# Kernel tuning notes

Measured on AMD Instinct MI355X. Metric: run time of the kernel, lower is better.

Reference implementation:

```python
import jax, jax.numpy as jnp
import numpy as np

T, N, H, I = 128, 1024, 512, 64


def _orthogonal(key, shape, dtype=jnp.float32):
    # mimic torch nn.init.orthogonal_ on a [rows, cols] matrix
    rows, cols = shape
    a = jax.random.normal(key, (max(rows, cols), min(rows, cols)), dtype=jnp.float32)
    q, r = jnp.linalg.qr(a)
    q = q * jnp.sign(jnp.diag(r))
    if rows < cols:
        q = q.T
    return q[:rows, :cols].astype(dtype)


def setup_inputs() -> dict:
    key = jax.random.key(0)
    k1, k2, k3, k4, k5, k6 = jax.random.split(key, 6)
    hxs = jax.random.normal(k1, (N, H), dtype=jnp.float32)
    gru_init = jax.random.normal(k2, (T * N, H), dtype=jnp.float32)
    masks = jax.random.uniform(k3, (T * N, 1), dtype=jnp.float32)
    prev_action_one_hot = jax.random.normal(k4, (T, N, I), dtype=jnp.float32)
    # GRUCell params: weight_ih [3H, I], weight_hh [3H, H] (orthogonal init), zero biases
    W_ih = _orthogonal(k5, (3 * H, I))
    W_hh = _orthogonal(k6, (3 * H, H))
    b_ih = jnp.zeros((3 * H,), dtype=jnp.float32)
    b_hh = jnp.zeros((3 * H,), dtype=jnp.float32)
    return {"hxs": hxs, "gru_init": gru_init, "masks": masks,
            "prev_action_one_hot": prev_action_one_hot,
            "W_ih": W_ih, "W_hh": W_hh, "b_ih": b_ih, "b_hh": b_hh}


def _gru_cell(x, h, W_ih, W_hh, b_ih, b_hh):
    # PyTorch GRUCell math; gate order in weights is r, z, n
    gi = x @ W_ih.T + b_ih          # [N, 3H]
    gh = h @ W_hh.T + b_hh          # [N, 3H]
    i_r, i_z, i_n = jnp.split(gi, 3, axis=-1)
    h_r, h_z, h_n = jnp.split(gh, 3, axis=-1)
    r = jax.nn.sigmoid(i_r + h_r)
    z = jax.nn.sigmoid(i_z + h_z)
    n = jnp.tanh(i_n + r * h_n)
    return (1.0 - z) * n + z * h


def reference(hxs, gru_init, masks, prev_action_one_hot, W_ih, W_hh, b_ih, b_hh):
    n = hxs.shape[0]
    t = gru_init.shape[0] // n
    m = masks.reshape(t, n, 1)
    # NOTE: the original computes hxs*m + gru_init*(1-m) per step but never uses it
    # (dead code), so gru_init does not enter the output.

    def step(h, inp):
        mi, xi = inp
        h_new = _gru_cell(xi * mi, h * mi, W_ih, W_hh, b_ih, b_hh)
        return h_new, h_new

    h_final, outs = jax.lax.scan(step, hxs, (m, prev_action_one_hot))
    x = outs.reshape(t * n, -1)
    return x, h_final
```

## Files before the change

### kernel.cpp

```cpp
#include <hip/hip_runtime.h>


#define T_STEPS 128
#define NBATCH  1024
#define HDIM    512
#define IDIM    64
#define KTOT    576
#define BM      64
#define BN      32
#define LDP     40

typedef _Float16 half8  __attribute__((ext_vector_type(8)));
typedef float    floatx4 __attribute__((ext_vector_type(4)));

__global__ void prep_w_kernel(const float* __restrict__ Whh,
                              const float* __restrict__ Wih,
                              _Float16* __restrict__ W16) {
    int idx = blockIdx.x * 256 + threadIdx.x;
    if (idx >= 1536 * KTOT) return;
    int c = idx / KTOT;
    int k = idx - c * KTOT;
    float v = (k < HDIM) ? Whh[c * HDIM + k] : Wih[c * IDIM + (k - HDIM)];
    W16[idx] = (_Float16)v;
}

__device__ __forceinline__ float sigmoidf_(float x) {
    return 1.0f / (1.0f + __expf(-x));
}

__global__ __launch_bounds__(256)
void gru_step_kernel(const float* __restrict__ h_prev,
                     const float* __restrict__ x_t,
                     const float* __restrict__ m_t,
                     const _Float16* __restrict__ W16,
                     const float* __restrict__ b_ih,
                     const float* __restrict__ b_hh,
                     float* __restrict__ out_x,
                     float* __restrict__ out_h) {
    __shared__ __align__(16) _Float16 As[BM * LDP];
    __shared__ __align__(16) _Float16 Bs[3][BN * LDP];

    const int tid = threadIdx.x;
    const int rt = blockIdx.x >> 4;
    const int ctile = blockIdx.x & 15;
    const int rowbase = rt * BM;
    const int colbase = ctile * BN;

    const int arow = tid >> 2;
    const int ak0  = (tid & 3) * 8;
    const float maskv = m_t[rowbase + arow];

    const int wave = tid >> 6;
    const int lane = tid & 63;
    const int n16  = lane & 15;
    const int q    = lane >> 4;

    floatx4 acc_r[2], acc_z[2], acc_hn[2], acc_in[2];
#pragma unroll
    for (int bt = 0; bt < 2; ++bt) {
        acc_r[bt] = (floatx4){0.f, 0.f, 0.f, 0.f};
        acc_z[bt] = (floatx4){0.f, 0.f, 0.f, 0.f};
        acc_hn[bt] = (floatx4){0.f, 0.f, 0.f, 0.f};
        acc_in[bt] = (floatx4){0.f, 0.f, 0.f, 0.f};
    }

    for (int kt = 0; kt < 18; ++kt) {
        const int kbase = kt * 32;

        const float* asrc;
        if (kt < 16) {
            asrc = h_prev + (size_t)(rowbase + arow) * HDIM + kbase + ak0;
        } else {
            asrc = x_t + (size_t)(rowbase + arow) * IDIM + (kbase - HDIM) + ak0;
        }
        floatx4 a0 = *(const floatx4*)asrc;
        floatx4 a1 = *(const floatx4*)(asrc + 4);
        half8 av;
        av[0] = (_Float16)(a0.x * maskv);
        av[1] = (_Float16)(a0.y * maskv);
        av[2] = (_Float16)(a0.z * maskv);
        av[3] = (_Float16)(a0.w * maskv);
        av[4] = (_Float16)(a1.x * maskv);
        av[5] = (_Float16)(a1.y * maskv);
        av[6] = (_Float16)(a1.z * maskv);
        av[7] = (_Float16)(a1.w * maskv);
        *(half8*)&As[arow * LDP + ak0] = av;

#pragma unroll
        for (int ii = 0; ii < 2; ++ii) {
            int idx = tid + ii * 256;
            if (idx < 384) {
                int g    = idx >> 7;
                int rem  = idx & 127;
                int brow = rem >> 2;
                int bk0  = (rem & 3) * 8;
                const _Float16* bsrc =
                    W16 + (size_t)(g * HDIM + colbase + brow) * KTOT + kbase + bk0;
                *(half8*)&Bs[g][brow * LDP + bk0] = *(const half8*)bsrc;
            }
        }
        __syncthreads();

        half8 af = *(const half8*)&As[(wave * 16 + n16) * LDP + q * 8];
#pragma unroll
        for (int bt = 0; bt < 2; ++bt) {
            half8 br = *(const half8*)&Bs[0][(bt * 16 + n16) * LDP + q * 8];
            half8 bz = *(const half8*)&Bs[1][(bt * 16 + n16) * LDP + q * 8];
            half8 bn = *(const half8*)&Bs[2][(bt * 16 + n16) * LDP + q * 8];
            acc_r[bt] = __builtin_amdgcn_mfma_f32_16x16x32_f16(af, br, acc_r[bt], 0, 0, 0);
            acc_z[bt] = __builtin_amdgcn_mfma_f32_16x16x32_f16(af, bz, acc_z[bt], 0, 0, 0);
            if (kt < 16) {
                acc_hn[bt] = __builtin_amdgcn_mfma_f32_16x16x32_f16(af, bn, acc_hn[bt], 0, 0, 0);
            } else {
                acc_in[bt] = __builtin_amdgcn_mfma_f32_16x16x32_f16(af, bn, acc_in[bt], 0, 0, 0);
            }
        }
        __syncthreads();
    }

#pragma unroll
    for (int bt = 0; bt < 2; ++bt) {
        const int c = colbase + bt * 16 + n16;
        const float brb = b_ih[c] + b_hh[c];
        const float bzb = b_ih[c + HDIM] + b_hh[c + HDIM];
        const float bin = b_ih[c + 2 * HDIM];
        const float bhn = b_hh[c + 2 * HDIM];
#pragma unroll
        for (int r = 0; r < 4; ++r) {
            const int i = rowbase + wave * 16 + q * 4 + r;
            const float rg = sigmoidf_(acc_r[bt][r] + brb);
            const float zg = sigmoidf_(acc_z[bt][r] + bzb);
            const float ng = tanhf(acc_in[bt][r] + bin + rg * (acc_hn[bt][r] + bhn));
            const float hm = h_prev[(size_t)i * HDIM + c] * m_t[i];
            const float hv = (1.0f - zg) * ng + zg * hm;
            out_x[(size_t)i * HDIM + c] = hv;
            if (out_h) out_h[(size_t)i * HDIM + c] = hv;
        }
    }
}

extern "C" void kernel_launch(void* const* d_in, const int* in_sizes, int n_in,
                              void* d_out, int out_size, void* d_ws, size_t ws_size,
                              hipStream_t stream) {
    const float* hxs   = (const float*)d_in[0];
    const float* masks = (const float*)d_in[2];
    const float* pact  = (const float*)d_in[3];
    const float* W_ih  = (const float*)d_in[4];
    const float* W_hh  = (const float*)d_in[5];
    const float* b_ih  = (const float*)d_in[6];
    const float* b_hh  = (const float*)d_in[7];
    float* out = (float*)d_out;
    _Float16* W16 = (_Float16*)d_ws;

    const int wtot = 1536 * KTOT;
    prep_w_kernel<<<(wtot + 255) / 256, 256, 0, stream>>>(W_hh, W_ih, W16);

    for (int t = 0; t < T_STEPS; ++t) {
        const float* h_prev =
            (t == 0) ? hxs : out + (size_t)(t - 1) * NBATCH * HDIM;
        float* out_x = out + (size_t)t * NBATCH * HDIM;
        float* out_h =
            (t == T_STEPS - 1) ? out + (size_t)T_STEPS * NBATCH * HDIM : nullptr;
        gru_step_kernel<<<256, 256, 0, stream>>>(
            h_prev, pact + (size_t)t * NBATCH * IDIM, masks + (size_t)t * NBATCH,
            W16, b_ih, b_hh, out_x, out_h);
    }
}
```

Baseline: 2.899 ms.

## Keep masked fp16 hidden state between steps and drop LDS staging in GRU step

Each step now writes the next step's hidden state already masked and converted to fp16 into a ping-pong buffer. The input actions are pre-masked and converted to fp16 once up front. The step kernel no longer stages through shared memory and has no barriers: each wave loads MFMA fragments straight from global memory and computes a 32x32 tile per gate, with weights as the A operand so outputs come out as contiguous 4-wide vectors. This removes the per-step fp32 reads, the conversions and the __syncthreads, at the cost of more workspace, uncoalesced direct global loads that rely on cache, and fewer threads per block.

```diff
diff --git a/kernel.cpp b/kernel.cpp
--- a/kernel.cpp
+++ b/kernel.cpp
@@ -6,11 +6,9 @@
 #define HDIM    512
 #define IDIM    64
 #define KTOT    576
-#define BM      64
-#define BN      32
-#define LDP     40
 
 typedef _Float16 half8  __attribute__((ext_vector_type(8)));
+typedef _Float16 half4  __attribute__((ext_vector_type(4)));
 typedef float    floatx4 __attribute__((ext_vector_type(4)));
 
 __global__ void prep_w_kernel(const float* __restrict__ Whh,
@@ -24,117 +22,165 @@
     W16[idx] = (_Float16)v;
 }
 
+__global__ void prep_x_kernel(const float* __restrict__ pact,
+                              const float* __restrict__ masks,
+                              _Float16* __restrict__ x16) {
+    int idx = blockIdx.x * 256 + threadIdx.x;
+    if (idx >= T_STEPS * NBATCH * IDIM / 4) return;
+    int e = idx * 4;
+    float mk = masks[e >> 6];
+    floatx4 v = *(const floatx4*)(pact + e);
+    half4 h;
+    h[0] = (_Float16)(v.x * mk);
+    h[1] = (_Float16)(v.y * mk);
+    h[2] = (_Float16)(v.z * mk);
+    h[3] = (_Float16)(v.w * mk);
+    *(half4*)(x16 + e) = h;
+}
+
+__global__ void prep_h_kernel(const float* __restrict__ hxs,
+                              const float* __restrict__ masks,
+                              _Float16* __restrict__ h16) {
+    int idx = blockIdx.x * 256 + threadIdx.x;
+    if (idx >= NBATCH * HDIM / 4) return;
+    int e = idx * 4;
+    float mk = masks[e >> 9];
+    floatx4 v = *(const floatx4*)(hxs + e);
+    half4 h;
+    h[0] = (_Float16)(v.x * mk);
+    h[1] = (_Float16)(v.y * mk);
+    h[2] = (_Float16)(v.z * mk);
+    h[3] = (_Float16)(v.w * mk);
+    *(half4*)(h16 + e) = h;
+}
+
 __device__ __forceinline__ float sigmoidf_(float x) {
     return 1.0f / (1.0f + __expf(-x));
 }
 
-__global__ __launch_bounds__(256)
+#define MFMA16(a, b, c) __builtin_amdgcn_mfma_f32_16x16x32_f16((a), (b), (c), 0, 0, 0)
+
+__global__ __launch_bounds__(128, 1)
 void gru_step_kernel(const float* __restrict__ h_prev,
-                     const float* __restrict__ x_t,
+                     const _Float16* __restrict__ h16,
+                     const _Float16* __restrict__ x16,
                      const float* __restrict__ m_t,
+                     const float* __restrict__ m_next,
                      const _Float16* __restrict__ W16,
                      const float* __restrict__ b_ih,
                      const float* __restrict__ b_hh,
                      float* __restrict__ out_x,
-                     float* __restrict__ out_h) {
-    __shared__ __align__(16) _Float16 As[BM * LDP];
-    __shared__ __align__(16) _Float16 Bs[3][BN * LDP];
-
-    const int tid = threadIdx.x;
-    const int rt = blockIdx.x >> 4;
-    const int ctile = blockIdx.x & 15;
-    const int rowbase = rt * BM;
-    const int colbase = ctile * BN;
-
-    const int arow = tid >> 2;
-    const int ak0  = (tid & 3) * 8;
-    const float maskv = m_t[rowbase + arow];
-
+                     float* __restrict__ out_h,
+                     _Float16* __restrict__ h16_next) {
+    const int tid  = threadIdx.x;
     const int wave = tid >> 6;
     const int lane = tid & 63;
     const int n16  = lane & 15;
     const int q    = lane >> 4;
-
-    floatx4 acc_r[2], acc_z[2], acc_hn[2], acc_in[2];
-#pragma unroll
-    for (int bt = 0; bt < 2; ++bt) {
-        acc_r[bt] = (floatx4){0.f, 0.f, 0.f, 0.f};
-        acc_z[bt] = (floatx4){0.f, 0.f, 0.f, 0.f};
-        acc_hn[bt] = (floatx4){0.f, 0.f, 0.f, 0.f};
-        acc_in[bt] = (floatx4){0.f, 0.f, 0.f, 0.f};
-    }
-
-    for (int kt = 0; kt < 18; ++kt) {
-        const int kbase = kt * 32;
-
-        const float* asrc;
-        if (kt < 16) {
-            asrc = h_prev + (size_t)(rowbase + arow) * HDIM + kbase + ak0;
-        } else {
-            asrc = x_t + (size_t)(rowbase + arow) * IDIM + (kbase - HDIM) + ak0;
+    const int rowbase = (blockIdx.x >> 4) * 64 + wave * 32;
+    const int colbase = (blockIdx.x & 15) * 32;
+
+    floatx4 acc_r[2][2], acc_z[2][2], acc_hn[2][2], acc_in[2][2];
+#pragma unroll
+    for (int rs = 0; rs < 2; ++rs)
+#pragma unroll
+        for (int cs = 0; cs < 2; ++cs) {
+            acc_r[rs][cs]  = (floatx4){0.f, 0.f, 0.f, 0.f};
+            acc_z[rs][cs]  = (floatx4){0.f, 0.f, 0.f, 0.f};
+            acc_hn[rs][cs] = (floatx4){0.f, 0.f, 0.f, 0.f};
+            acc_in[rs][cs] = (floatx4){0.f, 0.f, 0.f, 0.f};
         }
-        floatx4 a0 = *(const floatx4*)asrc;
-        floatx4 a1 = *(const floatx4*)(asrc + 4);
-        half8 av;
-        av[0] = (_Float16)(a0.x * maskv);
-        av[1] = (_Float16)(a0.y * maskv);
-        av[2] = (_Float16)(a0.z * maskv);
-        av[3] = (_Float16)(a0.w * maskv);
-        av[4] = (_Float16)(a1.x * maskv);
-        av[5] = (_Float16)(a1.y * maskv);
-        av[6] = (_Float16)(a1.z * maskv);
-        av[7] = (_Float16)(a1.w * maskv);
-        *(half8*)&As[arow * LDP + ak0] = av;
-
-#pragma unroll
-        for (int ii = 0; ii < 2; ++ii) {
-            int idx = tid + ii * 256;
-            if (idx < 384) {
-                int g    = idx >> 7;
-                int rem  = idx & 127;
-                int brow = rem >> 2;
-                int bk0  = (rem & 3) * 8;
-                const _Float16* bsrc =
-                    W16 + (size_t)(g * HDIM + colbase + brow) * KTOT + kbase + bk0;
-                *(half8*)&Bs[g][brow * LDP + bk0] = *(const half8*)bsrc;
+
+    const _Float16* hptr = h16 + (rowbase + n16) * HDIM + q * 8;
+    const _Float16* wptr = W16 + (colbase + n16) * KTOT + q * 8;
+
+#pragma unroll 4
+    for (int kt = 0; kt < 16; ++kt) {
+        half8 hf0 = *(const half8*)(hptr);
+        half8 hf1 = *(const half8*)(hptr + 16 * HDIM);
+        half8 wr0 = *(const half8*)(wptr);
+        half8 wr1 = *(const half8*)(wptr + 16 * KTOT);
+        half8 wz0 = *(const half8*)(wptr + HDIM * KTOT);
+        half8 wz1 = *(const half8*)(wptr + (HDIM + 16) * KTOT);
+        half8 wn0 = *(const half8*)(wptr + 2 * HDIM * KTOT);
+        half8 wn1 = *(const half8*)(wptr + (2 * HDIM + 16) * KTOT);
+        acc_r[0][0]  = MFMA16(wr0, hf0, acc_r[0][0]);
+        acc_r[0][1]  = MFMA16(wr1, hf0, acc_r[0][1]);
+        acc_r[1][0]  = MFMA16(wr0, hf1, acc_r[1][0]);
+        acc_r[1][1]  = MFMA16(wr1, hf1, acc_r[1][1]);
+        acc_z[0][0]  = MFMA16(wz0, hf0, acc_z[0][0]);
+        acc_z[0][1]  = MFMA16(wz1, hf0, acc_z[0][1]);
+        acc_z[1][0]  = MFMA16(wz0, hf1, acc_z[1][0]);
+        acc_z[1][1]  = MFMA16(wz1, hf1, acc_z[1][1]);
+        acc_hn[0][0] = MFMA16(wn0, hf0, acc_hn[0][0]);
+        acc_hn[0][1] = MFMA16(wn1, hf0, acc_hn[0][1]);
+        acc_hn[1][0] = MFMA16(wn0, hf1, acc_hn[1][0]);
+        acc_hn[1][1] = MFMA16(wn1, hf1, acc_hn[1][1]);
+        hptr += 32;
+        wptr += 32;
+    }
+
+    const _Float16* xptr = x16 + (rowbase + n16) * IDIM + q * 8;
+#pragma unroll
+    for (int kt = 0; kt < 2; ++kt) {
+        half8 hf0 = *(const half8*)(xptr);
+        half8 hf1 = *(const half8*)(xptr + 16 * IDIM);
+        half8 wr0 = *(const half8*)(wptr);
+        half8 wr1 = *(const half8*)(wptr + 16 * KTOT);
+        half8 wz0 = *(const half8*)(wptr + HDIM * KTOT);
+        half8 wz1 = *(const half8*)(wptr + (HDIM + 16) * KTOT);
+        half8 wn0 = *(const half8*)(wptr + 2 * HDIM * KTOT);
+        half8 wn1 = *(const half8*)(wptr + (2 * HDIM + 16) * KTOT);
+        acc_r[0][0]  = MFMA16(wr0, hf0, acc_r[0][0]);
+        acc_r[0][1]  = MFMA16(wr1, hf0, acc_r[0][1]);
+        acc_r[1][0]  = MFMA16(wr0, hf1, acc_r[1][0]);
+        acc_r[1][1]  = MFMA16(wr1, hf1, acc_r[1][1]);
+        acc_z[0][0]  = MFMA16(wz0, hf0, acc_z[0][0]);
+        acc_z[0][1]  = MFMA16(wz1, hf0, acc_z[0][1]);
+        acc_z[1][0]  = MFMA16(wz0, hf1, acc_z[1][0]);
+        acc_z[1][1]  = MFMA16(wz1, hf1, acc_z[1][1]);
+        acc_in[0][0] = MFMA16(wn0, hf0, acc_in[0][0]);
+        acc_in[0][1] = MFMA16(wn1, hf0, acc_in[0][1]);
+        acc_in[1][0] = MFMA16(wn0, hf1, acc_in[1][0]);
+        acc_in[1][1] = MFMA16(wn1, hf1, acc_in[1][1]);
+        xptr += 32;
+        wptr += 32;
+    }
+
+#pragma unroll
+    for (int rs = 0; rs < 2; ++rs) {
+        const int i = rowbase + rs * 16 + n16;
+        const float mtv = m_t[i];
+        const float mnv = m_next ? m_next[i] : 0.0f;
+#pragma unroll
+        for (int cs = 0; cs < 2; ++cs) {
+            const int c0 = colbase + cs * 16 + q * 4;
+            floatx4 bir = *(const floatx4*)(b_ih + c0);
+            floatx4 bhr = *(const floatx4*)(b_hh + c0);
+            floatx4 biz = *(const floatx4*)(b_ih + HDIM + c0);
+            floatx4 bhz = *(const floatx4*)(b_hh + HDIM + c0);
+            floatx4 bin = *(const floatx4*)(b_ih + 2 * HDIM + c0);
+            floatx4 bhn = *(const floatx4*)(b_hh + 2 * HDIM + c0);
+            floatx4 hp4 = *(const floatx4*)(h_prev + (size_t)i * HDIM + c0);
+            floatx4 hv;
+#pragma unroll
+            for (int r = 0; r < 4; ++r) {
+                const float rg = sigmoidf_(acc_r[rs][cs][r] + bir[r] + bhr[r]);
+                const float zg = sigmoidf_(acc_z[rs][cs][r] + biz[r] + bhz[r]);
+                const float ng = tanhf(acc_in[rs][cs][r] + bin[r] +
+                                       rg * (acc_hn[rs][cs][r] + bhn[r]));
+                hv[r] = (1.0f - zg) * ng + zg * (hp4[r] * mtv);
             }
-        }
-        __syncthreads();
-
-        half8 af = *(const half8*)&As[(wave * 16 + n16) * LDP + q * 8];
-#pragma unroll
-        for (int bt = 0; bt < 2; ++bt) {
-            half8 br = *(const half8*)&Bs[0][(bt * 16 + n16) * LDP + q * 8];
-            half8 bz = *(const half8*)&Bs[1][(bt * 16 + n16) * LDP + q * 8];
-            half8 bn = *(const half8*)&Bs[2][(bt * 16 + n16) * LDP + q * 8];
-            acc_r[bt] = __builtin_amdgcn_mfma_f32_16x16x32_f16(af, br, acc_r[bt], 0, 0, 0);
-            acc_z[bt] = __builtin_amdgcn_mfma_f32_16x16x32_f16(af, bz, acc_z[bt], 0, 0, 0);
-            if (kt < 16) {
-                acc_hn[bt] = __builtin_amdgcn_mfma_f32_16x16x32_f16(af, bn, acc_hn[bt], 0, 0, 0);
-            } else {
-                acc_in[bt] = __builtin_amdgcn_mfma_f32_16x16x32_f16(af, bn, acc_in[bt], 0, 0, 0);
+            *(floatx4*)(out_x + (size_t)i * HDIM + c0) = hv;
+            if (out_h) *(floatx4*)(out_h + (size_t)i * HDIM + c0) = hv;
+            if (m_next) {
+                half4 hh;
+                hh[0] = (_Float16)(hv[0] * mnv);
+                hh[1] = (_Float16)(hv[1] * mnv);
+                hh[2] = (_Float16)(hv[2] * mnv);
+                hh[3] = (_Float16)(hv[3] * mnv);
+                *(half4*)(h16_next + (size_t)i * HDIM + c0) = hh;
             }
-        }
-        __syncthreads();
-    }
-
-#pragma unroll
-    for (int bt = 0; bt < 2; ++bt) {
-        const int c = colbase + bt * 16 + n16;
-        const float brb = b_ih[c] + b_hh[c];
-        const float bzb = b_ih[c + HDIM] + b_hh[c + HDIM];
-        const float bin = b_ih[c + 2 * HDIM];
-        const float bhn = b_hh[c + 2 * HDIM];
-#pragma unroll
-        for (int r = 0; r < 4; ++r) {
-            const int i = rowbase + wave * 16 + q * 4 + r;
-            const float rg = sigmoidf_(acc_r[bt][r] + brb);
-            const float zg = sigmoidf_(acc_z[bt][r] + bzb);
-            const float ng = tanhf(acc_in[bt][r] + bin + rg * (acc_hn[bt][r] + bhn));
-            const float hm = h_prev[(size_t)i * HDIM + c] * m_t[i];
-            const float hv = (1.0f - zg) * ng + zg * hm;
-            out_x[(size_t)i * HDIM + c] = hv;
-            if (out_h) out_h[(size_t)i * HDIM + c] = hv;
         }
     }
 }
@@ -150,19 +196,32 @@
     const float* b_ih  = (const float*)d_in[6];
     const float* b_hh  = (const float*)d_in[7];
     float* out = (float*)d_out;
-    _Float16* W16 = (_Float16*)d_ws;
+
+    _Float16* W16  = (_Float16*)d_ws;
+    _Float16* x16  = W16 + 1536 * KTOT;
+    _Float16* h16a = x16 + (size_t)T_STEPS * NBATCH * IDIM;
+    _Float16* h16b = h16a + (size_t)NBATCH * HDIM;
 
     const int wtot = 1536 * KTOT;
     prep_w_kernel<<<(wtot + 255) / 256, 256, 0, stream>>>(W_hh, W_ih, W16);
+    const int xtot = T_STEPS * NBATCH * IDIM / 4;
+    prep_x_kernel<<<(xtot + 255) / 256, 256, 0, stream>>>(pact, masks, x16);
+    const int htot = NBATCH * HDIM / 4;
+    prep_h_kernel<<<(htot + 255) / 256, 256, 0, stream>>>(hxs, masks, h16a);
 
     for (int t = 0; t < T_STEPS; ++t) {
         const float* h_prev =
             (t == 0) ? hxs : out + (size_t)(t - 1) * NBATCH * HDIM;
+        const _Float16* hcur = (t & 1) ? h16b : h16a;
+        _Float16* hnext      = (t & 1) ? h16a : h16b;
+        const float* mnext =
+            (t < T_STEPS - 1) ? masks + (size_t)(t + 1) * NBATCH : nullptr;
         float* out_x = out + (size_t)t * NBATCH * HDIM;
         float* out_h =
             (t == T_STEPS - 1) ? out + (size_t)T_STEPS * NBATCH * HDIM : nullptr;
-        gru_step_kernel<<<256, 256, 0, stream>>>(
-            h_prev, pact + (size_t)t * NBATCH * IDIM, masks + (size_t)t * NBATCH,
-            W16, b_ih, b_hh, out_x, out_h);
-    }
-}
+        gru_step_kernel<<<256, 128, 0, stream>>>(
+            h_prev, hcur, x16 + (size_t)t * NBATCH * IDIM,
+            masks + (size_t)t * NBATCH, mnext, W16, b_ih, b_hh,
+            out_x, out_h, hnext);
+    }
+}
```

Result: faster. 2.368 ms (-18.3%).
